# Optimization experiments

Measured on AMD Instinct MI355X. Metric: run time of the kernel, lower is better.

The kernel has to match this reference:

```python
import jax, jax.numpy as jnp
from jax import lax
import numpy as np

V, E, H, B, S = 50000, 128, 64, 512, 512
OUT = 2


def _lstm_layer(x, Wih, Whh, bih, bhh):
    # x: [B, S, D]; Wih: [4H, D]; Whh: [4H, H]; PyTorch gate order i,f,g,o
    b = bih + bhh
    Bsz = x.shape[0]
    h0 = jnp.zeros((Bsz, H), x.dtype)
    c0 = jnp.zeros((Bsz, H), x.dtype)
    # precompute input projections for all timesteps (one big GEMM)
    xproj = jnp.einsum('bsd,gd->bsg', x, Wih) + b  # [B, S, 4H]

    def step(carry, xt):
        h, c = carry
        gates = xt + h @ Whh.T  # [B, 4H]
        i, f, g, o = jnp.split(gates, 4, axis=-1)
        i = jax.nn.sigmoid(i)
        f = jax.nn.sigmoid(f)
        g = jnp.tanh(g)
        o = jax.nn.sigmoid(o)
        c = f * c + i * g
        h = o * jnp.tanh(c)
        return (h, c), h

    (hT, cT), ys = lax.scan(step, (h0, c0), jnp.swapaxes(xproj, 0, 1))
    return jnp.swapaxes(ys, 0, 1), hT


def setup_inputs() -> dict:
    key = jax.random.key(0)
    ks = jax.random.split(key, 12)
    s = 0.05
    emb = jax.random.normal(ks[0], (V, E), jnp.float32) * s
    emb = emb.at[0].set(0.0)  # padding_idx=0
    inp = {
        'input_seq': jax.random.randint(ks[1], (B, S), 0, V, dtype=jnp.int64),
        'emb': emb,
        'Wih0': jax.random.normal(ks[2], (4 * H, E), jnp.float32) * s,
        'Whh0': jax.random.normal(ks[3], (4 * H, H), jnp.float32) * s,
        'bih0': jax.random.normal(ks[4], (4 * H,), jnp.float32) * s,
        'bhh0': jax.random.normal(ks[5], (4 * H,), jnp.float32) * s,
        'Wih1': jax.random.normal(ks[6], (4 * H, H), jnp.float32) * s,
        'Whh1': jax.random.normal(ks[7], (4 * H, H), jnp.float32) * s,
        'bih1': jax.random.normal(ks[8], (4 * H,), jnp.float32) * s,
        'bhh1': jax.random.normal(ks[9], (4 * H,), jnp.float32) * s,
        'Wfc': jax.random.normal(ks[10], (OUT, H), jnp.float32) * s,
        'bfc': jax.random.normal(ks[11], (OUT,), jnp.float32) * s,
    }
    return inp


def reference(input_seq, emb, Wih0, Whh0, bih0, bhh0, Wih1, Whh1, bih1, bhh1, Wfc, bfc):
    # eval-mode: dropouts are identity
    x = emb[input_seq]                       # [B, S, E] embedding lookup
    y0, h0T = _lstm_layer(x, Wih0, Whh0, bih0, bhh0)
    y1, h1T = _lstm_layer(y0, Wih1, Whh1, bih1, bhh1)
    out = jax.nn.sigmoid(h1T @ Wfc.T + bfc)  # [B, 2]
    return out
```

## Files before the change

### kernel.cpp

```cpp
#include <hip/hip_runtime.h>
#include <hip/hip_bf16.h>
#include <hip/hip_fp16.h>
#include <math.h>

#define Bv   512
#define Sv   512
#define Hv   64
#define Ev   128
#define G4   256
#define VV   50000
#define Rr   16
#define NTILE ((VV + 31) / 32)

typedef _Float16 f16;
typedef _Float16 f16x2 __attribute__((ext_vector_type(2)));
typedef _Float16 f16x4 __attribute__((ext_vector_type(4)));
typedef _Float16 f16x8 __attribute__((ext_vector_type(8)));
typedef float    f32x4 __attribute__((ext_vector_type(4)));

#if __has_builtin(__builtin_amdgcn_exp2f)
#define EXP2F(x) __builtin_amdgcn_exp2f(x)
#else
#define EXP2F(x) exp2f(x)
#endif
#if __has_builtin(__builtin_amdgcn_rcpf)
#define RCPF(x) __builtin_amdgcn_rcpf(x)
#else
#define RCPF(x) (1.0f / (x))
#endif
#define LOG2E 1.442695040888963f

__device__ __forceinline__ float fast_sigmoid(float x) {
    float e = EXP2F(-LOG2E * x);
    return RCPF(1.0f + e);
}

__device__ __forceinline__ f16x2 PK(float a, float b) {
    return __builtin_bit_cast(f16x2, __builtin_amdgcn_cvt_pkrtz(a, b));
}
__device__ __forceinline__ f16x2 C2(float c) {
    f16 h = (f16)c;
    return f16x2{h, h};
}
__device__ __forceinline__ f16x2 sig2(f16x2 x) {
    f16x2 x2 = x * x;
    f16x2 t = x2 * C2(2.08333333e-3f) + C2(-2.08333333e-2f);
    t = x2 * t + C2(0.25f);
    return x * t + C2(0.5f);
}
__device__ __forceinline__ f16x2 tanh2(f16x2 x) {
    f16x2 x2 = x * x;
    f16x2 t = x2 * C2(1.33333333e-1f) + C2(-3.33333333e-1f);
    t = x2 * t + C2(1.f);
    return x * t;
}

__device__ __forceinline__ void cell_update4(const f32x4 acc[4], f16x2 c2[2],
                                             f16* dst, int stride) {
#pragma unroll
    for (int p = 0; p < 2; ++p) {
        f16x2 ig = sig2 (PK(acc[0][2 * p], acc[0][2 * p + 1]));
        f16x2 fg = sig2 (PK(acc[1][2 * p], acc[1][2 * p + 1]));
        f16x2 gg = tanh2(PK(acc[2][2 * p], acc[2][2 * p + 1]));
        f16x2 og = sig2 (PK(acc[3][2 * p], acc[3][2 * p + 1]));
        c2[p] = fg * c2[p] + ig * gg;
        f16x2 hv = og * tanh2(c2[p]);
        dst[(2 * p) * stride]     = hv[0];
        dst[(2 * p + 1) * stride] = hv[1];
    }
}

__device__ __forceinline__ f16x8 cvt8(float4 a, float4 b) {
    f16x2 p0 = PK(a.x, a.y), p1 = PK(a.z, a.w);
    f16x2 p2 = PK(b.x, b.y), p3 = PK(b.z, b.w);
    f16x8 r;
    r[0] = p0[0]; r[1] = p0[1]; r[2] = p1[0]; r[3] = p1[1];
    r[4] = p2[0]; r[5] = p2[1]; r[6] = p3[0]; r[7] = p3[1];
    return r;
}

__global__ __launch_bounds__(256) void vocab_gemm_mfma(
    const float* __restrict__ emb,
    const float* __restrict__ Wih0,
    const float* __restrict__ bih0, const float* __restrict__ bhh0,
    f16* __restrict__ P2)
{
    const int tid  = threadIdx.x;
    const int w    = tid >> 6;
    const int lane = tid & 63;
    const int col  = lane & 15;
    const int quad = lane >> 4;
    const int u    = 16 * w + col;

    __shared__ __align__(16) f16 sA[32][136];

    const size_t m0 = (size_t)blockIdx.x * 32;

    const int sr = tid >> 3;
    const int sc = (tid & 7) * 16;
    size_t rg = m0 + sr;
    if (rg >= VV) rg = 0;
    const float4* ap = (const float4*)(emb + rg * (size_t)Ev + sc);
    float4 v0 = ap[0], v1 = ap[1], v2 = ap[2], v3 = ap[3];

    f16x8 Bf[4][4];
    float bb[4];
#pragma unroll
    for (int tt = 0; tt < 4; ++tt) {
        const int n = 64 * tt + u;
#pragma unroll
        for (int kc = 0; kc < 4; ++kc) {
            const float4* bp = (const float4*)(Wih0 + (size_t)n * Ev + kc * 32 + quad * 8);
            Bf[tt][kc] = cvt8(bp[0], bp[1]);
        }
        bb[tt] = bih0[n] + bhh0[n];
    }

    *(f16x8*)&sA[sr][sc]     = cvt8(v0, v1);
    *(f16x8*)&sA[sr][sc + 8] = cvt8(v2, v3);
    __syncthreads();

    f16x8 Af[2][4];
#pragma unroll
    for (int mh = 0; mh < 2; ++mh)
#pragma unroll
        for (int kc = 0; kc < 4; ++kc)
            Af[mh][kc] = *(const f16x8*)&sA[mh * 16 + col][kc * 32 + quad * 8];

    f32x4 acc[2][4];
#pragma unroll
    for (int mh = 0; mh < 2; ++mh)
#pragma unroll
        for (int tt = 0; tt < 4; ++tt) {
#pragma unroll
            for (int r = 0; r < 4; ++r) acc[mh][tt][r] = 0.f;
#pragma unroll
            for (int kc = 0; kc < 4; ++kc)
                acc[mh][tt] = __builtin_amdgcn_mfma_f32_16x16x32_f16(
                    Af[mh][kc], Bf[tt][kc], acc[mh][tt], 0, 0, 0);
        }

#pragma unroll
    for (int mh = 0; mh < 2; ++mh)
#pragma unroll
        for (int r = 0; r < 4; ++r) {
            size_t row = m0 + mh * 16 + quad * 4 + r;
            if (row < VV) {
                f16x4 pk;
#pragma unroll
                for (int tt = 0; tt < 4; ++tt)
                    pk[tt] = (f16)(acc[mh][tt][r] + bb[tt]);
                *(f16x4*)(P2 + row * (size_t)G4 + u * 4) = pk;
            }
        }
}

__device__ __forceinline__ void load_chunk(uint2 (&X)[4][4],
    const int (*idxl)[516], int rowbase, int sb, const f16* Pl2) {
    if (sb > Sv - 4) sb = Sv - 4;
#pragma unroll
    for (int r = 0; r < 4; ++r) {
        int4 v = *(const int4*)&idxl[rowbase + r][sb];
        X[r][0] = *(const uint2*)(Pl2 + (size_t)(unsigned)v.x * G4);
        X[r][1] = *(const uint2*)(Pl2 + (size_t)(unsigned)v.y * G4);
        X[r][2] = *(const uint2*)(Pl2 + (size_t)(unsigned)v.z * G4);
        X[r][3] = *(const uint2*)(Pl2 + (size_t)(unsigned)v.w * G4);
    }
}

__global__ __launch_bounds__(512) void lstm_mfma(
    const f16* __restrict__ P2,
    const int* __restrict__ idx,
    const float* __restrict__ Whh0,
    const float* __restrict__ Wih1,
    const float* __restrict__ Whh1,
    const float* __restrict__ bih1, const float* __restrict__ bhh1,
    const float* __restrict__ Wfc,
    const float* __restrict__ bfc,
    float* __restrict__ out)
{
    const int tid  = threadIdx.x;
    const int wave = tid >> 6;
    const int lane = tid & 63;
    const int grp  = wave >> 2;
    const int w    = wave & 3;
    const int col  = lane & 15;
    const int quad = lane >> 4;
    const int u    = 16 * w + col;
    const int rowbase = quad * 4;
    const int rb   = blockIdx.x * Rr;

    __shared__ __align__(16) f16 h0b[4][Rr][72];
    __shared__ __align__(16) f16 h1b[2][Rr][72];
    __shared__ __align__(16) int idxl[Rr][516];

    for (int k = tid; k < Rr * Sv; k += 512) {
        int r = k >> 9, s = k & 511;
        idxl[r][s] = idx[(size_t)(rb + r) * Sv + s];
    }
    for (int k = tid; k < 4 * Rr * 72; k += 512)
        (&h0b[0][0][0])[k] = (f16)0.f;
    for (int k = tid; k < 2 * Rr * 72; k += 512)
        (&h1b[0][0][0])[k] = (f16)0.f;

    f16x8 Bh[4][2];
    f16x8 Bi[4][2];
    f16x8 B1[4][2];
    f32x4 bgv[4];
    if (grp == 0) {
#pragma unroll
        for (int g = 0; g < 4; ++g) {
            const int n = u + 64 * g;
#pragma unroll
            for (int kt = 0; kt < 2; ++kt) {
                const float4* sp = (const float4*)(Whh0 + (size_t)n * Hv + kt * 32 + quad * 8);
                Bh[g][kt] = cvt8(sp[0], sp[1]);
            }
        }
    } else {
#pragma unroll
        for (int g = 0; g < 4; ++g) {
            const int n = u + 64 * g;
#pragma unroll
            for (int kt = 0; kt < 2; ++kt) {
                const float4* si = (const float4*)(Wih1 + (size_t)n * Hv + kt * 32 + quad * 8);
                const float4* s1 = (const float4*)(Whh1 + (size_t)n * Hv + kt * 32 + quad * 8);
                Bi[g][kt] = cvt8(si[0], si[1]);
                B1[g][kt] = cvt8(s1[0], s1[1]);
            }
            float b = bih1[n] + bhh1[n];
            bgv[g] = f32x4{b, b, b, b};
        }
    }

    f16x2 c2[2] = {C2(0.f), C2(0.f)};
    uint2 Xa[4][4], Xb[4][4];
    f16x8 pa0[2], pa1[2];
    const f16* Pl2 = P2 + u * 4;

    __syncthreads();

    if (grp == 0) load_chunk(Xa, idxl, rowbase, 0, Pl2);

    for (int o = 0; o < Sv / 8; ++o) {
        const int s0 = o * 8;
#pragma unroll
        for (int jj = 0; jj < 8; ++jj) {
            const int i = s0 + jj;
            if (grp == 0) {
                const int rp = (i + 3) & 3;
                const int wp = i & 3;
                f32x4 acc[4];
#pragma unroll
                for (int r = 0; r < 4; ++r) {
                    f16x4 xf = __builtin_bit_cast(f16x4,
                        (jj < 4) ? Xa[r][jj & 3] : Xb[r][jj & 3]);
#pragma unroll
                    for (int g = 0; g < 4; ++g) acc[g][r] = (float)xf[g];
                }
                if (jj == 0) load_chunk(Xb, idxl, rowbase, s0 + 4, Pl2);
                if (jj == 4) load_chunk(Xa, idxl, rowbase, s0 + 8, Pl2);
                f16x8 a0 = *(const f16x8*)&h0b[rp][col][quad * 8];
                f16x8 a1 = *(const f16x8*)&h0b[rp][col][32 + quad * 8];
#pragma unroll
                for (int g = 0; g < 4; ++g) {
                    acc[g] = __builtin_amdgcn_mfma_f32_16x16x32_f16(a0, Bh[g][0], acc[g], 0, 0, 0);
                    acc[g] = __builtin_amdgcn_mfma_f32_16x16x32_f16(a1, Bh[g][1], acc[g], 0, 0, 0);
                }
                cell_update4(acc, c2, &h0b[wp][rowbase][u], 72);
            } else {
                const int pu = i & 1;
                if (i >= 2) {
                    const int rs1 = (i + 1) & 1;
                    const int ws1 = i & 1;
                    f16x8 a10 = *(const f16x8*)&h1b[rs1][col][quad * 8];
                    f16x8 a11 = *(const f16x8*)&h1b[rs1][col][32 + quad * 8];
                    {
                        const int pf = (i + 3) & 3;
                        pa0[pu ^ 1] = *(const f16x8*)&h0b[pf][col][quad * 8];
                        pa1[pu ^ 1] = *(const f16x8*)&h0b[pf][col][32 + quad * 8];
                    }
                    f32x4 acc[4];
#pragma unroll
                    for (int g = 0; g < 4; ++g) {
                        f32x4 t = __builtin_amdgcn_mfma_f32_16x16x32_f16(pa0[pu], Bi[g][0], bgv[g], 0, 0, 0);
                        t = __builtin_amdgcn_mfma_f32_16x16x32_f16(pa1[pu], Bi[g][1], t, 0, 0, 0);
                        t = __builtin_amdgcn_mfma_f32_16x16x32_f16(a10, B1[g][0], t, 0, 0, 0);
                        acc[g] = __builtin_amdgcn_mfma_f32_16x16x32_f16(a11, B1[g][1], t, 0, 0, 0);
                    }
                    cell_update4(acc, c2, &h1b[ws1][rowbase][u], 72);
                } else if (i >= 1) {
                    const int pf = (i + 3) & 3;
                    pa0[pu ^ 1] = *(const f16x8*)&h0b[pf][col][quad * 8];
                    pa1[pu ^ 1] = *(const f16x8*)&h0b[pf][col][32 + quad * 8];
                }
            }
            __syncthreads();
        }
    }

    if (grp == 1) {
        f16x8 a10 = *(const f16x8*)&h1b[1][col][quad * 8];
        f16x8 a11 = *(const f16x8*)&h1b[1][col][32 + quad * 8];
        pa0[1] = *(const f16x8*)&h0b[3][col][quad * 8];
        pa1[1] = *(const f16x8*)&h0b[3][col][32 + quad * 8];
        f32x4 acc[4];
#pragma unroll
        for (int g = 0; g < 4; ++g) {
            f32x4 t = __builtin_amdgcn_mfma_f32_16x16x32_f16(pa0[0], Bi[g][0], bgv[g], 0, 0, 0);
            t = __builtin_amdgcn_mfma_f32_16x16x32_f16(pa1[0], Bi[g][1], t, 0, 0, 0);
            t = __builtin_amdgcn_mfma_f32_16x16x32_f16(a10, B1[g][0], t, 0, 0, 0);
            acc[g] = __builtin_amdgcn_mfma_f32_16x16x32_f16(a11, B1[g][1], t, 0, 0, 0);
        }
        cell_update4(acc, c2, &h1b[0][rowbase][u], 72);
    }
    __syncthreads();

    if (grp == 1) {
        f16x8 a10 = *(const f16x8*)&h1b[0][col][quad * 8];
        f16x8 a11 = *(const f16x8*)&h1b[0][col][32 + quad * 8];
        f32x4 acc[4];
#pragma unroll
        for (int g = 0; g < 4; ++g) {
            f32x4 t = __builtin_amdgcn_mfma_f32_16x16x32_f16(pa0[1], Bi[g][0], bgv[g], 0, 0, 0);
            t = __builtin_amdgcn_mfma_f32_16x16x32_f16(pa1[1], Bi[g][1], t, 0, 0, 0);
            t = __builtin_amdgcn_mfma_f32_16x16x32_f16(a10, B1[g][0], t, 0, 0, 0);
            acc[g] = __builtin_amdgcn_mfma_f32_16x16x32_f16(a11, B1[g][1], t, 0, 0, 0);
        }
        cell_update4(acc, c2, &h1b[1][rowbase][u], 72);
    }
    __syncthreads();

    if (tid < 2 * Rr) {
        const int r = tid >> 1, j = tid & 1;
        float s = bfc[j];
        const float* wf = Wfc + (size_t)j * Hv;
#pragma unroll 8
        for (int k = 0; k < Hv; ++k) s += (float)h1b[1][r][k] * wf[k];
        out[(size_t)(rb + r) * 2 + j] = fast_sigmoid(s);
    }
}

extern "C" void kernel_launch(void* const* d_in, const int* in_sizes, int n_in,
                              void* d_out, int out_size, void* d_ws, size_t ws_size,
                              hipStream_t stream)
{
    const int*   idx  = (const int*)  d_in[0];
    const float* emb  = (const float*)d_in[1];
    const float* Wih0 = (const float*)d_in[2];
    const float* Whh0 = (const float*)d_in[3];
    const float* bih0 = (const float*)d_in[4];
    const float* bhh0 = (const float*)d_in[5];
    const float* Wih1 = (const float*)d_in[6];
    const float* Whh1 = (const float*)d_in[7];
    const float* bih1 = (const float*)d_in[8];
    const float* bhh1 = (const float*)d_in[9];
    const float* Wfc  = (const float*)d_in[10];
    const float* bfc  = (const float*)d_in[11];
    float* out = (float*)d_out;

    f16* P2 = (f16*)d_ws;

    vocab_gemm_mfma<<<NTILE, 256, 0, stream>>>(emb, Wih0, bih0, bhh0, P2);
    lstm_mfma<<<Bv / Rr, 512, 0, stream>>>(P2, idx, Whh0,
                                           Wih1, Whh1, bih1, bhh1, Wfc, bfc, out);
}
```

Before: 387.9 us.

## Single-buffer LSTM hidden states with two barriers per timestep

Replaces the multi-slot ring buffers for layer-0 and layer-1 hidden states with single LDS buffers. Each timestep is split into a read/MMA phase and a write (cell update) phase separated by an extra barrier. Layer 1's input-projection MFMAs are issued before the first barrier and its recurrent MFMAs after it. This shrinks LDS use and removes the register-prefetched copies of h0, but it doubles the number of block-wide barriers on the serial recurrence path.

```diff
diff --git a/kernel.cpp b/kernel.cpp
--- a/kernel.cpp
+++ b/kernel.cpp
@@ -190,18 +190,18 @@
     const int rowbase = quad * 4;
     const int rb   = blockIdx.x * Rr;
 
-    __shared__ __align__(16) f16 h0b[4][Rr][72];
-    __shared__ __align__(16) f16 h1b[2][Rr][72];
+    __shared__ __align__(16) f16 h0b[Rr][72];
+    __shared__ __align__(16) f16 h1b[Rr][72];
     __shared__ __align__(16) int idxl[Rr][516];
 
     for (int k = tid; k < Rr * Sv; k += 512) {
         int r = k >> 9, s = k & 511;
         idxl[r][s] = idx[(size_t)(rb + r) * Sv + s];
     }
-    for (int k = tid; k < 4 * Rr * 72; k += 512)
-        (&h0b[0][0][0])[k] = (f16)0.f;
-    for (int k = tid; k < 2 * Rr * 72; k += 512)
-        (&h1b[0][0][0])[k] = (f16)0.f;
+    for (int k = tid; k < Rr * 72; k += 512) {
+        (&h0b[0][0])[k] = (f16)0.f;
+        (&h1b[0][0])[k] = (f16)0.f;
+    }
 
     f16x8 Bh[4][2];
     f16x8 Bi[4][2];
@@ -235,7 +235,9 @@
 
     f16x2 c2[2] = {C2(0.f), C2(0.f)};
     uint2 Xa[4][4], Xb[4][4];
-    f16x8 pa0[2], pa1[2];
+    f32x4 acc0[4];
+    f32x4 acc1[4];
+    f32x4 tg[4];
     const f16* Pl2 = P2 + u * 4;
 
     __syncthreads();
@@ -248,87 +250,74 @@
         for (int jj = 0; jj < 8; ++jj) {
             const int i = s0 + jj;
             if (grp == 0) {
-                const int rp = (i + 3) & 3;
-                const int wp = i & 3;
-                f32x4 acc[4];
 #pragma unroll
                 for (int r = 0; r < 4; ++r) {
                     f16x4 xf = __builtin_bit_cast(f16x4,
                         (jj < 4) ? Xa[r][jj & 3] : Xb[r][jj & 3]);
 #pragma unroll
-                    for (int g = 0; g < 4; ++g) acc[g][r] = (float)xf[g];
+                    for (int g = 0; g < 4; ++g) acc0[g][r] = (float)xf[g];
                 }
                 if (jj == 0) load_chunk(Xb, idxl, rowbase, s0 + 4, Pl2);
                 if (jj == 4) load_chunk(Xa, idxl, rowbase, s0 + 8, Pl2);
-                f16x8 a0 = *(const f16x8*)&h0b[rp][col][quad * 8];
-                f16x8 a1 = *(const f16x8*)&h0b[rp][col][32 + quad * 8];
+                f16x8 a0 = *(const f16x8*)&h0b[col][quad * 8];
+                f16x8 a1 = *(const f16x8*)&h0b[col][32 + quad * 8];
 #pragma unroll
                 for (int g = 0; g < 4; ++g) {
-                    acc[g] = __builtin_amdgcn_mfma_f32_16x16x32_f16(a0, Bh[g][0], acc[g], 0, 0, 0);
-                    acc[g] = __builtin_amdgcn_mfma_f32_16x16x32_f16(a1, Bh[g][1], acc[g], 0, 0, 0);
+                    acc0[g] = __builtin_amdgcn_mfma_f32_16x16x32_f16(a0, Bh[g][0], acc0[g], 0, 0, 0);
+                    acc0[g] = __builtin_amdgcn_mfma_f32_16x16x32_f16(a1, Bh[g][1], acc0[g], 0, 0, 0);
                 }
-                cell_update4(acc, c2, &h0b[wp][rowbase][u], 72);
             } else {
-                const int pu = i & 1;
-                if (i >= 2) {
-                    const int rs1 = (i + 1) & 1;
-                    const int ws1 = i & 1;
-                    f16x8 a10 = *(const f16x8*)&h1b[rs1][col][quad * 8];
-                    f16x8 a11 = *(const f16x8*)&h1b[rs1][col][32 + quad * 8];
-                    {
-                        const int pf = (i + 3) & 3;
-                        pa0[pu ^ 1] = *(const f16x8*)&h0b[pf][col][quad * 8];
-                        pa1[pu ^ 1] = *(const f16x8*)&h0b[pf][col][32 + quad * 8];
+                if (i >= 2)
+                    cell_update4(acc1, c2, &h1b[rowbase][u], 72);
+                if (i >= 1) {
+                    f16x8 pa0 = *(const f16x8*)&h0b[col][quad * 8];
+                    f16x8 pa1 = *(const f16x8*)&h0b[col][32 + quad * 8];
+#pragma unroll
+                    for (int g = 0; g < 4; ++g) {
+                        tg[g] = __builtin_amdgcn_mfma_f32_16x16x32_f16(pa0, Bi[g][0], bgv[g], 0, 0, 0);
+                        tg[g] = __builtin_amdgcn_mfma_f32_16x16x32_f16(pa1, Bi[g][1], tg[g], 0, 0, 0);
                     }
-                    f32x4 acc[4];
-#pragma unroll
-                    for (int g = 0; g < 4; ++g) {
-                        f32x4 t = __builtin_amdgcn_mfma_f32_16x16x32_f16(pa0[pu], Bi[g][0], bgv[g], 0, 0, 0);
-                        t = __builtin_amdgcn_mfma_f32_16x16x32_f16(pa1[pu], Bi[g][1], t, 0, 0, 0);
-                        t = __builtin_amdgcn_mfma_f32_16x16x32_f16(a10, B1[g][0], t, 0, 0, 0);
-                        acc[g] = __builtin_amdgcn_mfma_f32_16x16x32_f16(a11, B1[g][1], t, 0, 0, 0);
-                    }
-                    cell_update4(acc, c2, &h1b[ws1][rowbase][u], 72);
-                } else if (i >= 1) {
-                    const int pf = (i + 3) & 3;
-                    pa0[pu ^ 1] = *(const f16x8*)&h0b[pf][col][quad * 8];
-                    pa1[pu ^ 1] = *(const f16x8*)&h0b[pf][col][32 + quad * 8];
                 }
             }
             __syncthreads();
+            if (grp == 0) {
+                cell_update4(acc0, c2, &h0b[rowbase][u], 72);
+            } else if (i >= 1) {
+                f16x8 a10 = *(const f16x8*)&h1b[col][quad * 8];
+                f16x8 a11 = *(const f16x8*)&h1b[col][32 + quad * 8];
+#pragma unroll
+                for (int g = 0; g < 4; ++g) {
+                    f32x4 t = __builtin_amdgcn_mfma_f32_16x16x32_f16(a10, B1[g][0], tg[g], 0, 0, 0);
+                    acc1[g] = __builtin_amdgcn_mfma_f32_16x16x32_f16(a11, B1[g][1], t, 0, 0, 0);
+                }
+            }
+            __syncthreads();
         }
     }
 
     if (grp == 1) {
-        f16x8 a10 = *(const f16x8*)&h1b[1][col][quad * 8];
-        f16x8 a11 = *(const f16x8*)&h1b[1][col][32 + quad * 8];
-        pa0[1] = *(const f16x8*)&h0b[3][col][quad * 8];
-        pa1[1] = *(const f16x8*)&h0b[3][col][32 + quad * 8];
-        f32x4 acc[4];
+        cell_update4(acc1, c2, &h1b[rowbase][u], 72);
+        f16x8 pa0 = *(const f16x8*)&h0b[col][quad * 8];
+        f16x8 pa1 = *(const f16x8*)&h0b[col][32 + quad * 8];
 #pragma unroll
         for (int g = 0; g < 4; ++g) {
-            f32x4 t = __builtin_amdgcn_mfma_f32_16x16x32_f16(pa0[0], Bi[g][0], bgv[g], 0, 0, 0);
-            t = __builtin_amdgcn_mfma_f32_16x16x32_f16(pa1[0], Bi[g][1], t, 0, 0, 0);
-            t = __builtin_amdgcn_mfma_f32_16x16x32_f16(a10, B1[g][0], t, 0, 0, 0);
-            acc[g] = __builtin_amdgcn_mfma_f32_16x16x32_f16(a11, B1[g][1], t, 0, 0, 0);
-        }
-        cell_update4(acc, c2, &h1b[0][rowbase][u], 72);
-    }
-    __syncthreads();
-
+            tg[g] = __builtin_amdgcn_mfma_f32_16x16x32_f16(pa0, Bi[g][0], bgv[g], 0, 0, 0);
+            tg[g] = __builtin_amdgcn_mfma_f32_16x16x32_f16(pa1, Bi[g][1], tg[g], 0, 0, 0);
+        }
+    }
+    __syncthreads();
     if (grp == 1) {
-        f16x8 a10 = *(const f16x8*)&h1b[0][col][quad * 8];
-        f16x8 a11 = *(const f16x8*)&h1b[0][col][32 + quad * 8];
-        f32x4 acc[4];
+        f16x8 a10 = *(const f16x8*)&h1b[col][quad * 8];
+        f16x8 a11 = *(const f16x8*)&h1b[col][32 + quad * 8];
 #pragma unroll
         for (int g = 0; g < 4; ++g) {
-            f32x4 t = __builtin_amdgcn_mfma_f32_16x16x32_f16(pa0[1], Bi[g][0], bgv[g], 0, 0, 0);
-            t = __builtin_amdgcn_mfma_f32_16x16x32_f16(pa1[1], Bi[g][1], t, 0, 0, 0);
-            t = __builtin_amdgcn_mfma_f32_16x16x32_f16(a10, B1[g][0], t, 0, 0, 0);
-            acc[g] = __builtin_amdgcn_mfma_f32_16x16x32_f16(a11, B1[g][1], t, 0, 0, 0);
-        }
-        cell_update4(acc, c2, &h1b[1][rowbase][u], 72);
-    }
+            f32x4 t = __builtin_amdgcn_mfma_f32_16x16x32_f16(a10, B1[g][0], tg[g], 0, 0, 0);
+            acc1[g] = __builtin_amdgcn_mfma_f32_16x16x32_f16(a11, B1[g][1], t, 0, 0, 0);
+        }
+    }
+    __syncthreads();
+    if (grp == 1)
+        cell_update4(acc1, c2, &h1b[rowbase][u], 72);
     __syncthreads();
 
     if (tid < 2 * Rr) {
@@ -336,7 +325,7 @@
         float s = bfc[j];
         const float* wf = Wfc + (size_t)j * Hv;
 #pragma unroll 8
-        for (int k = 0; k < Hv; ++k) s += (float)h1b[1][r][k] * wf[k];
+        for (int k = 0; k < Hv; ++k) s += (float)h1b[r][k] * wf[k];
         out[(size_t)(rb + r) * 2 + j] = fast_sigmoid(s);
     }
 }
```

New measurement: 457.2 us. 1.18x slower.
